# Kernel optimization log

Measured on AMD Instinct MI355X. Metric: run time of the kernel, lower is better.

## Reference

```python
import jax, jax.numpy as jnp
import numpy as np

N = 100000
HID = 256
NCLASS = 64
DIMS = [334, 512, 128, 745, 256, 600]
TAU = 1.0
BN_EPS = 1e-5


def setup_inputs() -> dict:
    key = jax.random.key(0)
    ks = jax.random.split(key, 32)
    inp = {}
    for i, d in enumerate(DIMS):
        inp[f"feat{i}"] = jax.random.normal(ks[i], (N, d), dtype=jnp.float32)
        inp[f"emb{i}"] = jax.random.uniform(ks[8 + i], (d, HID), minval=-0.5, maxval=0.5, dtype=jnp.float32)
    for j in range(2):
        inp[f"lab{j}"] = jax.random.normal(ks[6 + j], (N, NCLASS), dtype=jnp.float32)
        inp[f"lemb{j}"] = jax.random.uniform(ks[16 + j], (NCLASS, HID), minval=-0.5, maxval=0.5, dtype=jnp.float32)
    inp["alpha"] = jnp.ones((8,), jnp.float32)
    inp["gumbels"] = jax.random.gumbel(ks[20], (8,), dtype=jnp.float32)  # -log(Exp(1)) noise
    inp["prelu_a"] = jnp.asarray(0.25, jnp.float32)
    # xavier-ish init for the output head (gain for relu)
    inp["w_out"] = jax.random.normal(ks[21], (NCLASS, HID), dtype=jnp.float32) * np.float32(np.sqrt(2.0 / (HID + NCLASS)))
    inp["epoch_sampled"] = jnp.arange(8, dtype=jnp.int32)
    return inp


def reference(feat0, feat1, feat2, feat3, feat4, feat5, lab0, lab1,
              emb0, emb1, emb2, emb3, emb4, emb5, lemb0, lemb1,
              alpha, gumbels, prelu_a, w_out, epoch_sampled):
    feats = [feat0, feat1, feat2, feat3, feat4, feat5, lab0, lab1]
    embs = [emb0, emb1, emb2, emb3, emb4, emb5, lemb0, lemb1]
    # Gumbel-softmax gate over the sampled meta-path channels (soft probs used by forward)
    ws = alpha[epoch_sampled]
    logits = (jax.nn.log_softmax(ws, axis=-1) + gumbels) / TAU
    probs = jax.nn.softmax(logits, axis=-1)  # [8]
    # weighted combine of per-key projections; avoids materializing [N, 8, HID]
    x = probs[0] * (feats[0] @ embs[0])  # [N, HID]
    for c in range(1, 8):
        x = x + probs[c] * (feats[c] @ embs[c])
    # PReLU (single shared slope)
    h = jnp.where(x >= 0, x, prelu_a * x)
    # Linear(hidden -> nclass, no bias) + BatchNorm1d(affine=False, batch stats)
    z = h @ w_out.T  # [N, NCLASS]
    mean = jnp.mean(z, axis=0)
    var = jnp.mean((z - mean) ** 2, axis=0)  # biased variance, as torch BN
    return (z - mean) * jax.lax.rsqrt(var + BN_EPS)
```

## Files before the change

kernel.cpp:

```cpp
#include <hip/hip_runtime.h>

#define N_ROWS 100000
#define HID 256
#define NCLASS 64
#define KPAD 2816
#define NTILE 44
#define BN_EPS 1e-5f

typedef unsigned short u16;
typedef __bf16 bf16x8 __attribute__((ext_vector_type(8)));
typedef float floatx4 __attribute__((ext_vector_type(4)));
typedef float f32x4u __attribute__((ext_vector_type(4), aligned(4)));

union FragU { bf16x8 v; uint4 u; u16 s[8]; };
union BfBits { __bf16 b; u16 s; };

struct GemmArgs {
    const float* feat[8];
    const float* emb[8];
};

__constant__ int c_POFF[9] = {0, 384, 896, 1024, 1792, 2048, 2688, 2752, 2816};
__constant__ int c_KDIM[8] = {334, 512, 128, 745, 256, 600, 64, 64};

__global__ void k_prep0(const float* __restrict__ alpha, const float* __restrict__ gumbels,
                        const int* __restrict__ es, float* __restrict__ wsf) {
    int tid = threadIdx.x;
    if (tid < 128) wsf[8 + tid] = 0.f;
    if (tid == 0) {
        float w[8], mx = -1e30f;
        for (int i = 0; i < 8; ++i) { w[i] = alpha[es[i]]; mx = fmaxf(mx, w[i]); }
        float se = 0.f;
        for (int i = 0; i < 8; ++i) se += expf(w[i] - mx);
        float lse = logf(se) + mx;
        float t[8], mt = -1e30f;
        for (int i = 0; i < 8; ++i) { t[i] = (w[i] - lse + gumbels[i]); mt = fmaxf(mt, t[i]); }
        float p[8], ss = 0.f;
        for (int i = 0; i < 8; ++i) { p[i] = expf(t[i] - mt); ss += p[i]; }
        for (int i = 0; i < 8; ++i) wsf[i] = p[i] / ss;
    }
}

__global__ __launch_bounds__(256) void k_prep1(GemmArgs ga, const float* __restrict__ w_out,
                                               const float* __restrict__ wsf,
                                               u16* __restrict__ WcT, u16* __restrict__ wT) {
    int bx = blockIdx.x, tid = threadIdx.x;
    if (bx < KPAD) {
        int kp = bx, n = tid;
        int c = 0;
        #pragma unroll
        for (int i = 1; i < 8; ++i) c += (kp >= c_POFF[i]);
        int l = kp - c_POFF[c];
        float v = 0.f;
        if (l < c_KDIM[c]) v = wsf[c] * ga.emb[c][l * HID + n];
        BfBits u; u.b = (__bf16)v;
        WcT[n * KPAD + kp] = u.s;
    } else {
        int cls = bx - KPAD;
        BfBits u; u.b = (__bf16)w_out[cls * HID + tid];
        wT[cls * HID + tid] = u.s;
    }
}

__global__ __launch_bounds__(256) void k_gemm1(GemmArgs ga, const u16* __restrict__ WcT,
                                               const u16* __restrict__ wT,
                                               const float* __restrict__ prelu_a,
                                               float* __restrict__ out,
                                               float* __restrict__ gstats) {
    __shared__ __align__(16) char smA[8192];
    __shared__ __align__(16) char smB[32768];
    __shared__ float sstats[128];

    const int tid = threadIdx.x;
    const int lane = tid & 63;
    const int quad = lane >> 4;
    const int l15 = lane & 15;
    const int wave = tid >> 6;
    const int row0 = blockIdx.x * 64;

    if (tid < 128) sstats[tid] = 0.f;

    floatx4 acc[4][4];
    #pragma unroll
    for (int i = 0; i < 4; ++i)
        #pragma unroll
        for (int j = 0; j < 4; ++j)
            acc[i][j] = (floatx4){0.f, 0.f, 0.f, 0.f};

    for (int t = 0; t < NTILE; ++t) {
        const int k0 = t * 64;
        int c = 0;
        #pragma unroll
        for (int i = 1; i < 8; ++i) c += (k0 >= c_POFF[i]);
        const int Kc = c_KDIM[c];
        const int lkb = k0 - c_POFF[c];
        const float* fp_base = ga.feat[c];

        #pragma unroll
        for (int i = 0; i < 2; ++i) {
            int o = tid + i * 256;
            int row = o >> 3, oct = o & 7;
            int r = row0 + row;
            int lk = lkb + oct * 8;
            const float* fp = fp_base + r * Kc + lk;
            float vv[8];
            if (r < N_ROWS && lk + 8 <= Kc) {
                f32x4u a0 = *(const f32x4u*)fp;
                f32x4u a1 = *(const f32x4u*)(fp + 4);
                vv[0] = a0.x; vv[1] = a0.y; vv[2] = a0.z; vv[3] = a0.w;
                vv[4] = a1.x; vv[5] = a1.y; vv[6] = a1.z; vv[7] = a1.w;
            } else {
                #pragma unroll
                for (int j = 0; j < 8; ++j)
                    vv[j] = (r < N_ROWS && lk + j < Kc) ? fp[j] : 0.f;
            }
            FragU f;
            #pragma unroll
            for (int j = 0; j < 8; ++j) f.v[j] = (__bf16)vv[j];
            *(uint4*)(smA + row * 128 + ((oct ^ (row & 7)) << 4)) = f.u;
        }

        const u16* WcTk = WcT + k0;
        #pragma unroll
        for (int it = 0; it < 8; ++it) {
            int ci = tid + it * 256;
            int n = ci >> 3, osl = ci & 7;
            int osrc = osl ^ (n & 7);
            uint4 d = *(const uint4*)(WcTk + n * KPAD + osrc * 8);
            *(uint4*)(smB + ci * 16) = d;
        }
        __syncthreads();

        #pragma unroll
        for (int ks = 0; ks < 2; ++ks) {
            int oct = ks * 4 + quad;
            FragU af[4], bfr[4];
            #pragma unroll
            for (int mf = 0; mf < 4; ++mf) {
                int m = mf * 16 + l15;
                af[mf].u = *(const uint4*)(smA + m * 128 + ((oct ^ (m & 7)) << 4));
            }
            #pragma unroll
            for (int nf = 0; nf < 4; ++nf) {
                int n = wave * 64 + nf * 16 + l15;
                bfr[nf].u = *(const uint4*)(smB + n * 128 + ((oct ^ (n & 7)) << 4));
            }
            #pragma unroll
            for (int mf = 0; mf < 4; ++mf)
                #pragma unroll
                for (int nf = 0; nf < 4; ++nf)
                    acc[mf][nf] = __builtin_amdgcn_mfma_f32_16x16x32_bf16(
                        af[mf].v, bfr[nf].v, acc[mf][nf], 0, 0, 0);
        }
        __syncthreads();
    }

    const float slope = prelu_a[0];
    #pragma unroll
    for (int nf = 0; nf < 4; ++nf) {
        int colg = wave * 64 + nf * 16 + l15;
        int oct = colg >> 3, sub = colg & 7;
        #pragma unroll
        for (int mf = 0; mf < 4; ++mf) {
            #pragma unroll
            for (int r = 0; r < 4; ++r) {
                int row = mf * 16 + quad * 4 + r;
                float x = acc[mf][nf][r];
                float hx = x >= 0.f ? x : slope * x;
                BfBits u; u.b = (__bf16)hx;
                *(u16*)(smB + row * 512 + ((oct ^ (row & 7)) << 4) + sub * 2) = u.s;
            }
        }
    }
    __syncthreads();

    floatx4 acc2[4];
    #pragma unroll
    for (int i = 0; i < 4; ++i) acc2[i] = (floatx4){0.f, 0.f, 0.f, 0.f};
    {
        int m = wave * 16 + l15;
        #pragma unroll
        for (int ks = 0; ks < 8; ++ks) {
            int oct = ks * 4 + quad;
            FragU ah;
            ah.u = *(const uint4*)(smB + m * 512 + ((oct ^ (m & 7)) << 4));
            #pragma unroll
            for (int nf = 0; nf < 4; ++nf) {
                int cls = nf * 16 + l15;
                FragU bw;
                bw.u = *(const uint4*)(wT + cls * HID + oct * 8);
                acc2[nf] = __builtin_amdgcn_mfma_f32_16x16x32_bf16(ah.v, bw.v, acc2[nf], 0, 0, 0);
            }
        }
    }

    #pragma unroll
    for (int nf = 0; nf < 4; ++nf) {
        int cls = nf * 16 + l15;
        float s1 = 0.f, s2 = 0.f;
        #pragma unroll
        for (int r = 0; r < 4; ++r) {
            int row = wave * 16 + quad * 4 + r;
            int grow = row0 + row;
            float z = acc2[nf][r];
            if (grow < N_ROWS) out[grow * NCLASS + cls] = z;
            s1 += z; s2 += z * z;
        }
        s1 += __shfl_xor(s1, 16); s1 += __shfl_xor(s1, 32);
        s2 += __shfl_xor(s2, 16); s2 += __shfl_xor(s2, 32);
        if (quad == 0) {
            atomicAdd(&sstats[cls], s1);
            atomicAdd(&sstats[64 + cls], s2);
        }
    }
    __syncthreads();
    if (tid < 128) atomicAdd(&gstats[tid], sstats[tid]);
}

__global__ void k_stats(float* __restrict__ wsf) {
    int c = threadIdx.x;
    if (c < 64) {
        float s1 = wsf[8 + c], s2 = wsf[8 + 64 + c];
        float mean = s1 * (1.f / N_ROWS);
        float var = s2 * (1.f / N_ROWS) - mean * mean;
        wsf[8 + c] = mean;
        wsf[8 + 64 + c] = rsqrtf(var + BN_EPS);
    }
}

__global__ __launch_bounds__(256) void k_norm(float* __restrict__ out, const float* __restrict__ wsf) {
    int idx = blockIdx.x * 256 + threadIdx.x;
    int base = idx * 4;
    int c0 = base & 63;
    floatx4 v = *(floatx4*)(out + base);
    #pragma unroll
    for (int j = 0; j < 4; ++j) {
        float mean = wsf[8 + c0 + j];
        float inv  = wsf[72 + c0 + j];
        v[j] = (v[j] - mean) * inv;
    }
    *(floatx4*)(out + base) = v;
}

extern "C" void kernel_launch(void* const* d_in, const int* in_sizes, int n_in,
                              void* d_out, int out_size, void* d_ws, size_t ws_size,
                              hipStream_t stream) {
    GemmArgs ga;
    const int fidx[8] = {0, 2, 4, 6, 8, 10, 12, 14};
    const int eidx[8] = {1, 3, 5, 7, 9, 11, 13, 15};
    for (int i = 0; i < 8; ++i) {
        ga.feat[i] = (const float*)d_in[fidx[i]];
        ga.emb[i]  = (const float*)d_in[eidx[i]];
    }
    const float* alpha   = (const float*)d_in[16];
    const float* gumbels = (const float*)d_in[17];
    const float* prelu_a = (const float*)d_in[18];
    const float* w_out   = (const float*)d_in[19];
    const int*   es      = (const int*)d_in[20];

    float* wsf = (float*)d_ws;
    u16* WcT = (u16*)((char*)d_ws + 1024);
    u16* wT  = (u16*)((char*)d_ws + 1024 + (size_t)KPAD * 256 * 2);
    float* out = (float*)d_out;

    k_prep0<<<1, 256, 0, stream>>>(alpha, gumbels, es, wsf);
    k_prep1<<<KPAD + NCLASS, 256, 0, stream>>>(ga, w_out, wsf, WcT, wT);
    k_gemm1<<<(N_ROWS + 63) / 64, 256, 0, stream>>>(ga, WcT, wT, prelu_a, out, wsf + 8);
    k_stats<<<1, 64, 0, stream>>>(wsf);
    k_norm<<<(N_ROWS * NCLASS) / 1024, 256, 0, stream>>>(out, wsf);
}
```

Before: 1.106 ms.

## Double-buffer GEMM tiles with register prefetch and direct global-to-LDS weight loads

The combined weight matrix is now stored pre-tiled and pre-swizzled per K-tile, so each tile can be copied into LDS with global_load_lds 16-byte transfers that bypass registers. The main GEMM loop double-buffers LDS: it prefetches the next feature tile into registers and issues the next weight tile's async copy before the current tile's MFMAs. It then converts and stores the features after compute, leaving one barrier per iteration. LDS use grows to 80KB per block, which may reduce occupancy, and the prep kernel now runs far fewer blocks that each do strided reads.

```diff
diff --git a/kernel.cpp b/kernel.cpp
--- a/kernel.cpp
+++ b/kernel.cpp
@@ -8,6 +8,7 @@
 #define BN_EPS 1e-5f
 
 typedef unsigned short u16;
+typedef unsigned int u32;
 typedef __bf16 bf16x8 __attribute__((ext_vector_type(8)));
 typedef float floatx4 __attribute__((ext_vector_type(4)));
 typedef float f32x4u __attribute__((ext_vector_type(4), aligned(4)));
@@ -22,6 +23,11 @@
 
 __constant__ int c_POFF[9] = {0, 384, 896, 1024, 1792, 2048, 2688, 2752, 2816};
 __constant__ int c_KDIM[8] = {334, 512, 128, 745, 256, 600, 64, 64};
+
+__device__ __forceinline__ void gll16(const void* g, void* l) {
+    __builtin_amdgcn_global_load_lds((const __attribute__((address_space(1))) u32*)g,
+                                     (__attribute__((address_space(3))) u32*)l, 16, 0, 0);
+}
 
 __global__ void k_prep0(const float* __restrict__ alpha, const float* __restrict__ gumbels,
                         const int* __restrict__ es, float* __restrict__ wsf) {
@@ -43,33 +49,46 @@
 
 __global__ __launch_bounds__(256) void k_prep1(GemmArgs ga, const float* __restrict__ w_out,
                                                const float* __restrict__ wsf,
-                                               u16* __restrict__ WcT, u16* __restrict__ wT) {
-    int bx = blockIdx.x, tid = threadIdx.x;
-    if (bx < KPAD) {
-        int kp = bx, n = tid;
+                                               u16* __restrict__ WcTpre, u16* __restrict__ wT) {
+    const int t = blockIdx.x, n = threadIdx.x;
+    if (t < NTILE) {
         int c = 0;
         #pragma unroll
-        for (int i = 1; i < 8; ++i) c += (kp >= c_POFF[i]);
-        int l = kp - c_POFF[c];
-        float v = 0.f;
-        if (l < c_KDIM[c]) v = wsf[c] * ga.emb[c][l * HID + n];
-        BfBits u; u.b = (__bf16)v;
-        WcT[n * KPAD + kp] = u.s;
+        for (int i = 1; i < 8; ++i) c += (t * 64 >= c_POFF[i]);
+        const int Kc = c_KDIM[c];
+        const int lb = t * 64 - c_POFF[c];
+        const float sc = wsf[c];
+        const float* ep = ga.emb[c] + n;
+        u16* dst = WcTpre + t * 16384 + n * 64;
+        #pragma unroll
+        for (int slot = 0; slot < 8; ++slot) {
+            const int q8 = slot ^ (n & 7);
+            FragU f;
+            #pragma unroll
+            for (int j = 0; j < 8; ++j) {
+                const int l = lb + q8 * 8 + j;
+                float v = (l < Kc) ? sc * ep[l * HID] : 0.f;
+                f.v[j] = (__bf16)v;
+            }
+            ((uint4*)dst)[slot] = f.u;
+        }
     } else {
-        int cls = bx - KPAD;
-        BfBits u; u.b = (__bf16)w_out[cls * HID + tid];
-        wT[cls * HID + tid] = u.s;
-    }
-}
-
-__global__ __launch_bounds__(256) void k_gemm1(GemmArgs ga, const u16* __restrict__ WcT,
+        #pragma unroll 4
+        for (int cls = 0; cls < 64; ++cls) {
+            BfBits u; u.b = (__bf16)w_out[cls * HID + n];
+            wT[cls * HID + n] = u.s;
+        }
+    }
+}
+
+__global__ __launch_bounds__(256) void k_gemm1(GemmArgs ga, const u16* __restrict__ WcTpre,
                                                const u16* __restrict__ wT,
                                                const float* __restrict__ prelu_a,
                                                float* __restrict__ out,
                                                float* __restrict__ gstats) {
-    __shared__ __align__(16) char smA[8192];
-    __shared__ __align__(16) char smB[32768];
-    __shared__ float sstats[128];
+    __shared__ __align__(16) char sm[81920];
+    #define SMA(b) (sm + (b) * 8192)
+    #define SMB(b) (sm + 16384 + (b) * 32768)
 
     const int tid = threadIdx.x;
     const int lane = tid & 63;
@@ -78,8 +97,6 @@
     const int wave = tid >> 6;
     const int row0 = blockIdx.x * 64;
 
-    if (tid < 128) sstats[tid] = 0.f;
-
     floatx4 acc[4][4];
     #pragma unroll
     for (int i = 0; i < 4; ++i)
@@ -87,22 +104,15 @@
         for (int j = 0; j < 4; ++j)
             acc[i][j] = (floatx4){0.f, 0.f, 0.f, 0.f};
 
-    for (int t = 0; t < NTILE; ++t) {
-        const int k0 = t * 64;
-        int c = 0;
-        #pragma unroll
-        for (int i = 1; i < 8; ++i) c += (k0 >= c_POFF[i]);
-        const int Kc = c_KDIM[c];
-        const int lkb = k0 - c_POFF[c];
-        const float* fp_base = ga.feat[c];
-
+    {
+        const int Kc = c_KDIM[0];
+        const float* fpb = ga.feat[0];
         #pragma unroll
         for (int i = 0; i < 2; ++i) {
             int o = tid + i * 256;
             int row = o >> 3, oct = o & 7;
-            int r = row0 + row;
-            int lk = lkb + oct * 8;
-            const float* fp = fp_base + r * Kc + lk;
+            int r = row0 + row, lk = oct * 8;
+            const float* fp = fpb + r * Kc + lk;
             float vv[8];
             if (r < N_ROWS && lk + 8 <= Kc) {
                 f32x4u a0 = *(const f32x4u*)fp;
@@ -117,33 +127,70 @@
             FragU f;
             #pragma unroll
             for (int j = 0; j < 8; ++j) f.v[j] = (__bf16)vv[j];
-            *(uint4*)(smA + row * 128 + ((oct ^ (row & 7)) << 4)) = f.u;
-        }
-
-        const u16* WcTk = WcT + k0;
+            *(uint4*)(SMA(0) + row * 128 + ((oct ^ (row & 7)) << 4)) = f.u;
+        }
+        const u16* src = WcTpre;
         #pragma unroll
         for (int it = 0; it < 8; ++it) {
             int ci = tid + it * 256;
-            int n = ci >> 3, osl = ci & 7;
-            int osrc = osl ^ (n & 7);
-            uint4 d = *(const uint4*)(WcTk + n * KPAD + osrc * 8);
-            *(uint4*)(smB + ci * 16) = d;
-        }
-        __syncthreads();
-
+            gll16(src + ci * 8, SMB(0) + ci * 16);
+        }
+    }
+    __syncthreads();
+
+    float pv[2][8];
+    for (int t = 0; t < NTILE; ++t) {
+        const int cur = t & 1, nxt = cur ^ 1;
+        const bool hn = (t + 1 < NTILE);
+
+        if (hn) {
+            const int k0n = (t + 1) * 64;
+            int cn = 0;
+            #pragma unroll
+            for (int i = 1; i < 8; ++i) cn += (k0n >= c_POFF[i]);
+            const int Kcn = c_KDIM[cn];
+            const int lkbn = k0n - c_POFF[cn];
+            const float* fpb = ga.feat[cn];
+            #pragma unroll
+            for (int i = 0; i < 2; ++i) {
+                int o = tid + i * 256;
+                int row = o >> 3, oct = o & 7;
+                int r = row0 + row, lk = lkbn + oct * 8;
+                const float* fp = fpb + r * Kcn + lk;
+                if (r < N_ROWS && lk + 8 <= Kcn) {
+                    f32x4u a0 = *(const f32x4u*)fp;
+                    f32x4u a1 = *(const f32x4u*)(fp + 4);
+                    pv[i][0] = a0.x; pv[i][1] = a0.y; pv[i][2] = a0.z; pv[i][3] = a0.w;
+                    pv[i][4] = a1.x; pv[i][5] = a1.y; pv[i][6] = a1.z; pv[i][7] = a1.w;
+                } else {
+                    #pragma unroll
+                    for (int j = 0; j < 8; ++j)
+                        pv[i][j] = (r < N_ROWS && lk + j < Kcn) ? fp[j] : 0.f;
+                }
+            }
+            const u16* src = WcTpre + (t + 1) * 16384;
+            #pragma unroll
+            for (int it = 0; it < 8; ++it) {
+                int ci = tid + it * 256;
+                gll16(src + ci * 8, SMB(nxt) + ci * 16);
+            }
+        }
+
+        const char* sA = SMA(cur);
+        const char* sB = SMB(cur);
         #pragma unroll
         for (int ks = 0; ks < 2; ++ks) {
-            int oct = ks * 4 + quad;
+            const int oct = ks * 4 + quad;
             FragU af[4], bfr[4];
             #pragma unroll
             for (int mf = 0; mf < 4; ++mf) {
                 int m = mf * 16 + l15;
-                af[mf].u = *(const uint4*)(smA + m * 128 + ((oct ^ (m & 7)) << 4));
+                af[mf].u = *(const uint4*)(sA + m * 128 + ((oct ^ (m & 7)) << 4));
             }
             #pragma unroll
             for (int nf = 0; nf < 4; ++nf) {
                 int n = wave * 64 + nf * 16 + l15;
-                bfr[nf].u = *(const uint4*)(smB + n * 128 + ((oct ^ (n & 7)) << 4));
+                bfr[nf].u = *(const uint4*)(sB + n * 128 + ((oct ^ (n & 7)) << 4));
             }
             #pragma unroll
             for (int mf = 0; mf < 4; ++mf)
@@ -152,10 +199,23 @@
                     acc[mf][nf] = __builtin_amdgcn_mfma_f32_16x16x32_bf16(
                         af[mf].v, bfr[nf].v, acc[mf][nf], 0, 0, 0);
         }
+
+        if (hn) {
+            #pragma unroll
+            for (int i = 0; i < 2; ++i) {
+                int o = tid + i * 256;
+                int row = o >> 3, oct = o & 7;
+                FragU f;
+                #pragma unroll
+                for (int j = 0; j < 8; ++j) f.v[j] = (__bf16)pv[i][j];
+                *(uint4*)(SMA(nxt) + row * 128 + ((oct ^ (row & 7)) << 4)) = f.u;
+            }
+        }
         __syncthreads();
     }
 
     const float slope = prelu_a[0];
+    char* hbuf = SMB(0);
     #pragma unroll
     for (int nf = 0; nf < 4; ++nf) {
         int colg = wave * 64 + nf * 16 + l15;
@@ -168,10 +228,12 @@
                 float x = acc[mf][nf][r];
                 float hx = x >= 0.f ? x : slope * x;
                 BfBits u; u.b = (__bf16)hx;
-                *(u16*)(smB + row * 512 + ((oct ^ (row & 7)) << 4) + sub * 2) = u.s;
-            }
-        }
-    }
+                *(u16*)(hbuf + row * 512 + ((oct ^ (row & 7)) << 4) + sub * 2) = u.s;
+            }
+        }
+    }
+    float* sstats = (float*)sm;
+    if (tid < 128) sstats[tid] = 0.f;
     __syncthreads();
 
     floatx4 acc2[4];
@@ -183,7 +245,7 @@
         for (int ks = 0; ks < 8; ++ks) {
             int oct = ks * 4 + quad;
             FragU ah;
-            ah.u = *(const uint4*)(smB + m * 512 + ((oct ^ (m & 7)) << 4));
+            ah.u = *(const uint4*)(hbuf + m * 512 + ((oct ^ (m & 7)) << 4));
             #pragma unroll
             for (int nf = 0; nf < 4; ++nf) {
                 int cls = nf * 16 + l15;
@@ -215,6 +277,8 @@
     }
     __syncthreads();
     if (tid < 128) atomicAdd(&gstats[tid], sstats[tid]);
+    #undef SMA
+    #undef SMB
 }
 
 __global__ void k_stats(float* __restrict__ wsf) {
@@ -259,13 +323,13 @@
     const int*   es      = (const int*)d_in[20];
 
     float* wsf = (float*)d_ws;
-    u16* WcT = (u16*)((char*)d_ws + 1024);
-    u16* wT  = (u16*)((char*)d_ws + 1024 + (size_t)KPAD * 256 * 2);
+    u16* WcTpre = (u16*)((char*)d_ws + 1024);
+    u16* wT  = (u16*)((char*)d_ws + 1024 + (size_t)NTILE * 16384 * 2);
     float* out = (float*)d_out;
 
     k_prep0<<<1, 256, 0, stream>>>(alpha, gumbels, es, wsf);
-    k_prep1<<<KPAD + NCLASS, 256, 0, stream>>>(ga, w_out, wsf, WcT, wT);
-    k_gemm1<<<(N_ROWS + 63) / 64, 256, 0, stream>>>(ga, WcT, wT, prelu_a, out, wsf + 8);
+    k_prep1<<<NTILE + 1, 256, 0, stream>>>(ga, w_out, wsf, WcTpre, wT);
+    k_gemm1<<<(N_ROWS + 63) / 64, 256, 0, stream>>>(ga, WcTpre, wT, prelu_a, out, wsf + 8);
     k_stats<<<1, 64, 0, stream>>>(wsf);
     k_norm<<<(N_ROWS * NCLASS) / 1024, 256, 0, stream>>>(out, wsf);
 }
```

New measurement: 1.041 ms. -5.9%, faster.
